# Kernel tuning notes

Measured on AMD Instinct MI355X. Metric: run time of the kernel, lower is better.

## Reference

```python
import jax, jax.numpy as jnp
import numpy as np

NUM_USERS = 100_000
NUM_ITEMS = 50_000
N_TOTAL = 150_100
EMBED_DIM = 64
NUM_LAYERS = 3
N_EDGES = 3_000_000
BATCH = 4096


def setup_inputs() -> dict:
    key = jax.random.key(0)
    k1, k2, k3, k4, k5, k6 = jax.random.split(key, 6)
    node_emb = jax.random.normal(k1, (N_TOTAL, EMBED_DIM), dtype=jnp.float32) * 0.1
    # COO sparse normalized adjacency (static irregular pattern)
    adj_row = jax.random.randint(k2, (N_EDGES,), 0, N_TOTAL, dtype=jnp.int32)
    adj_col = jax.random.randint(k3, (N_EDGES,), 0, N_TOTAL, dtype=jnp.int32)
    adj_val = jax.random.uniform(k4, (N_EDGES,), dtype=jnp.float32) * 0.05
    user_ids = jax.random.randint(k5, (BATCH,), 0, NUM_USERS, dtype=jnp.int32)
    item_ids = jax.random.randint(k6, (BATCH,), 0, NUM_ITEMS, dtype=jnp.int32)
    return {"node_emb": node_emb, "adj_val": adj_val, "adj_row": adj_row,
            "adj_col": adj_col, "user_ids": user_ids, "item_ids": item_ids}


def reference(node_emb, adj_val, adj_row, adj_col, user_ids, item_ids):
    # LightGCN propagation: K sparse SpMM layers, running mean over K+1 embeddings
    emb = node_emb                       # [N, D] layer-0
    acc = emb                            # running sum instead of stack+mean
    for _ in range(NUM_LAYERS):
        # SpMM: out[r] += val * emb[c]   (COO scatter-add)
        msgs = adj_val[:, None] * emb[adj_col]          # [E, D]
        emb = jax.ops.segment_sum(msgs, adj_row, num_segments=N_TOTAL)
        acc = acc + emb
    final = acc / jnp.float32(NUM_LAYERS + 1)           # mean over layers
    users = final[:NUM_USERS]
    items = final[NUM_USERS:NUM_USERS + NUM_ITEMS]
    u = users[user_ids]                                 # [B, D]
    i = items[item_ids]                                 # [B, D]
    return (u * i).sum(axis=-1)                         # [B]
```

## Files before the change

kernel.cpp:

```cpp
#include <hip/hip_runtime.h>

#define N_TOTAL    150100
#define NUM_USERS  100000
#define DIM        64
#define BSHIFT     8
#define BROWS      (1 << BSHIFT)
#define NBUK       ((N_TOTAL + BROWS - 1) / BROWS)
#define EPB        4096
#define CAP        5632
#define RSP        260

#define VSCALE     262144.0f
#define VINV       (1.0f / 262144.0f)

__device__ __forceinline__ int wave_incl_scan(int x, int lane) {
    #pragma unroll
    for (int off = 1; off < 64; off <<= 1) {
        int y = __shfl_up(x, off, 64);
        if (lane >= off) x += y;
    }
    return x;
}

__device__ __forceinline__ float ub0(unsigned w) { return (float)(w & 0xFFu); }
__device__ __forceinline__ float ub1(unsigned w) { return (float)((w >> 8) & 0xFFu); }
__device__ __forceinline__ float ub2(unsigned w) { return (float)((w >> 16) & 0xFFu); }
__device__ __forceinline__ float ub3(unsigned w) { return (float)(w >> 24); }

__device__ __forceinline__ unsigned quant_pack(float4 f, float inv) {
    int a = __float2int_rn(f.x * inv) + 128;
    int b = __float2int_rn(f.y * inv) + 128;
    int c = __float2int_rn(f.z * inv) + 128;
    int d = __float2int_rn(f.w * inv) + 128;
    a = min(max(a, 0), 255); b = min(max(b, 0), 255);
    c = min(max(c, 0), 255); d = min(max(d, 0), 255);
    return (unsigned)a | ((unsigned)b << 8) | ((unsigned)c << 16) | ((unsigned)d << 24);
}

__global__ void convert_quant(const float4* __restrict__ in4,
                              unsigned* __restrict__ q, float* __restrict__ sc,
                              int* __restrict__ gcount) {
    int t = blockIdx.x * blockDim.x + threadIdx.x;
    if (t < NBUK) gcount[t] = 0;
    int r = t >> 4, sl = t & 15;
    if (r >= N_TOTAL) return;
    float4 f = in4[(size_t)r * 16 + sl];
    float m = fmaxf(fmaxf(fabsf(f.x), fabsf(f.y)), fmaxf(fabsf(f.z), fabsf(f.w)));
    #pragma unroll
    for (int off = 1; off < 16; off <<= 1) m = fmaxf(m, __shfl_xor(m, off, 64));
    float inv = (m > 1e-30f) ? 127.0f / m : 0.0f;
    q[(size_t)r * 16 + sl] = quant_pack(f, inv);
    if (sl == 0) sc[r] = m * (1.0f / 127.0f);
}

__global__ void __launch_bounds__(256) fill_buckets(
        const int* __restrict__ rows, const int* __restrict__ cols,
        const float* __restrict__ vals, int n_edges,
        int* __restrict__ gcount,
        unsigned* __restrict__ epk, unsigned char* __restrict__ erow) {
    __shared__ unsigned      buf[EPB];
    __shared__ unsigned char rowb[EPB];
    __shared__ short         tgtb[EPB];
    __shared__ int hist[NBUK];
    __shared__ int pref[NBUK];
    __shared__ int cur[NBUK];
    __shared__ int loc[NBUK];
    __shared__ int wtot[4];
    const int tid = threadIdx.x;
    const int lane = tid & 63, wid = tid >> 6;
    const int base = blockIdx.x * EPB;
    int end = base + EPB; if (end > n_edges) end = n_edges;
    const int cnt = end - base;

    for (int i = tid; i < NBUK; i += 256) hist[i] = 0;
    __syncthreads();
    for (int i = base + tid; i < end; i += 256)
        atomicAdd(&hist[rows[i] >> BSHIFT], 1);
    __syncthreads();
    for (int b = tid; b < NBUK; b += 256) {
        int h = hist[b];
        loc[b] = h ? atomicAdd(&gcount[b], h) : 0;
    }
    const int t0 = tid * 3;
    int t1 = t0 + 3; if (t1 > NBUK) t1 = NBUK;
    int s = 0;
    for (int i = t0; i < t1; ++i) s += hist[i];
    int incl = wave_incl_scan(s, lane);
    if (lane == 63) wtot[wid] = incl;
    __syncthreads();
    int wofs = 0;
    for (int w = 0; w < wid; ++w) wofs += wtot[w];
    int run = incl + wofs - s;
    for (int i = t0; i < t1; ++i) {
        int h = hist[i];
        pref[i] = run;
        cur[i] = run;
        run += h;
    }
    __syncthreads();
    for (int i = base + tid; i < end; i += 256) {
        int r = rows[i];
        int b = r >> BSHIFT;
        int pos = atomicAdd(&cur[b], 1);
        int q = (int)(vals[i] * VSCALE + 0.5f);
        if (q > 16383) q = 16383;
        buf[pos]  = ((unsigned)cols[i] << 14) | (unsigned)q;
        rowb[pos] = (unsigned char)(r & (BROWS - 1));
        tgtb[pos] = (short)b;
    }
    __syncthreads();
    for (int i = tid; i < cnt; i += 256) {
        int b = tgtb[i];
        int o = loc[b] + (i - pref[b]);
        if (o < CAP) {
            int g = b * CAP + o;
            epk[g]  = buf[i];
            erow[g] = rowb[i];
        }
    }
}

__global__ void __launch_bounds__(256) bucket_sort(
        unsigned* __restrict__ epk,
        const unsigned char* __restrict__ erow,
        const int* __restrict__ gcount,
        int* __restrict__ rs) {
    __shared__ unsigned buf[CAP];
    __shared__ int hist[BROWS];
    __shared__ int curl[BROWS];
    __shared__ int wtot[4];
    const int tid = threadIdx.x;
    const int lane = tid & 63, wid = tid >> 6;
    const int b = blockIdx.x;
    const int k0 = b * CAP;
    int cnt = gcount[b]; if (cnt > CAP) cnt = CAP;

    hist[tid] = 0;
    __syncthreads();
    for (int i = tid; i < cnt; i += 256) {
        buf[i] = epk[k0 + i];
        atomicAdd(&hist[erow[k0 + i]], 1);
    }
    __syncthreads();
    int s = hist[tid];
    int incl = wave_incl_scan(s, lane);
    if (lane == 63) wtot[wid] = incl;
    __syncthreads();
    int wofs = 0;
    for (int w = 0; w < wid; ++w) wofs += wtot[w];
    int ex = incl + wofs - s;
    const int rbase = b << BSHIFT;
    int nrow = N_TOTAL - rbase; if (nrow > BROWS) nrow = BROWS;
    if (tid < nrow) rs[b * RSP + tid] = k0 + ex;
    if (tid == 0) rs[b * RSP + nrow] = k0 + cnt;
    curl[tid] = ex;
    __syncthreads();
    for (int i = tid; i < cnt; i += 256) {
        int rl = erow[k0 + i];
        int pos = atomicAdd(&curl[rl], 1);
        epk[k0 + pos] = buf[i];
    }
}


__global__ void spmm_q8(const unsigned* __restrict__ qt,
                        const float* __restrict__ sc,
                        const int* __restrict__ rs,
                        const unsigned* __restrict__ epk,
                        unsigned* __restrict__ qo,
                        float* __restrict__ so) {
    int t = blockIdx.x * blockDim.x + threadIdx.x;
    int r = t >> 4;
    int sl = t & 15;
    int lane = threadIdx.x & 63;
    int subbase = lane & 48;
    if (r >= N_TOTAL) return;
    const int* rsb = rs + (r >> BSHIFT) * RSP + (r & (BROWS - 1));
    int k0 = rsb[0], k1 = rsb[1];
    float4 s = make_float4(0.f, 0.f, 0.f, 0.f);
    float corr = 0.f;
    for (int kb = k0; kb < k1; kb += 16) {
        int cnt = k1 - kb; if (cnt > 16) cnt = 16;
        unsigned pr = (sl < cnt) ? epk[kb + sl] : 0u;
        int j = 0;
        for (; j + 4 <= cnt; j += 4) {
            unsigned e0 = (unsigned)__shfl((int)pr, subbase + j + 0, 64);
            unsigned e1 = (unsigned)__shfl((int)pr, subbase + j + 1, 64);
            unsigned e2 = (unsigned)__shfl((int)pr, subbase + j + 2, 64);
            unsigned e3 = (unsigned)__shfl((int)pr, subbase + j + 3, 64);
            int c0 = e0 >> 14, c1 = e1 >> 14, c2 = e2 >> 14, c3 = e3 >> 14;
            unsigned w0 = qt[(size_t)c0 * 16 + sl];
            unsigned w1 = qt[(size_t)c1 * 16 + sl];
            unsigned w2 = qt[(size_t)c2 * 16 + sl];
            unsigned w3 = qt[(size_t)c3 * 16 + sl];
            float vs0 = (float)(e0 & 16383u) * VINV * sc[c0];
            float vs1 = (float)(e1 & 16383u) * VINV * sc[c1];
            float vs2 = (float)(e2 & 16383u) * VINV * sc[c2];
            float vs3 = (float)(e3 & 16383u) * VINV * sc[c3];
            corr += vs0 + vs1 + vs2 + vs3;
            s.x += vs0 * ub0(w0); s.y += vs0 * ub1(w0);
            s.z += vs0 * ub2(w0); s.w += vs0 * ub3(w0);
            s.x += vs1 * ub0(w1); s.y += vs1 * ub1(w1);
            s.z += vs1 * ub2(w1); s.w += vs1 * ub3(w1);
            s.x += vs2 * ub0(w2); s.y += vs2 * ub1(w2);
            s.z += vs2 * ub2(w2); s.w += vs2 * ub3(w2);
            s.x += vs3 * ub0(w3); s.y += vs3 * ub1(w3);
            s.z += vs3 * ub2(w3); s.w += vs3 * ub3(w3);
        }
        for (; j < cnt; ++j) {
            unsigned e = (unsigned)__shfl((int)pr, subbase + j, 64);
            int c = e >> 14;
            unsigned w = qt[(size_t)c * 16 + sl];
            float vs = (float)(e & 16383u) * VINV * sc[c];
            corr += vs;
            s.x += vs * ub0(w); s.y += vs * ub1(w);
            s.z += vs * ub2(w); s.w += vs * ub3(w);
        }
    }
    float c128 = 128.0f * corr;
    s.x -= c128; s.y -= c128; s.z -= c128; s.w -= c128;
    float m = fmaxf(fmaxf(fabsf(s.x), fabsf(s.y)), fmaxf(fabsf(s.z), fabsf(s.w)));
    #pragma unroll
    for (int off = 1; off < 16; off <<= 1) m = fmaxf(m, __shfl_xor(m, off, 64));
    float inv = (m > 1e-30f) ? 127.0f / m : 0.0f;
    qo[(size_t)r * 16 + sl] = quant_pack(s, inv);
    if (sl == 0) so[r] = m * (1.0f / 127.0f);
}

__device__ __forceinline__ float4 dec4(unsigned w, float s) {
    return make_float4(s * (ub0(w) - 128.0f), s * (ub1(w) - 128.0f),
                       s * (ub2(w) - 128.0f), s * (ub3(w) - 128.0f));
}

__device__ __forceinline__ float4 rowsum_q8(const unsigned* __restrict__ qt,
                                            const float* __restrict__ sc,
                                            const int* __restrict__ rs,
                                            const unsigned* __restrict__ epk,
                                            int r, int sl, int subbase) {
    const int* rsb = rs + (r >> BSHIFT) * RSP + (r & (BROWS - 1));
    int k0 = rsb[0], k1 = rsb[1];
    float4 s = make_float4(0.f, 0.f, 0.f, 0.f);
    float corr = 0.f;
    for (int kb = k0; kb < k1; kb += 16) {
        int cnt = k1 - kb; if (cnt > 16) cnt = 16;
        unsigned pr = (sl < cnt) ? epk[kb + sl] : 0u;
        for (int j = 0; j < cnt; ++j) {
            unsigned e = (unsigned)__shfl((int)pr, subbase + j, 64);
            int c = e >> 14;
            unsigned w = qt[(size_t)c * 16 + sl];
            float vs = (float)(e & 16383u) * VINV * sc[c];
            corr += vs;
            s.x += vs * ub0(w); s.y += vs * ub1(w);
            s.z += vs * ub2(w); s.w += vs * ub3(w);
        }
    }
    float c128 = 128.0f * corr;
    s.x -= c128; s.y -= c128; s.z -= c128; s.w -= c128;
    return s;
}

__global__ void final_dot_fused(const float4* __restrict__ emb4,
                                const unsigned* __restrict__ q1,
                                const float* __restrict__ s1,
                                const unsigned* __restrict__ q2,
                                const float* __restrict__ s2,
                                const int* __restrict__ rs,
                                const unsigned* __restrict__ epk,
                                const int* __restrict__ user_ids,
                                const int* __restrict__ item_ids,
                                float* __restrict__ out, int batch) {
    int t = blockIdx.x * blockDim.x + threadIdx.x;
    int b = t >> 4, sl = t & 15;
    int lane = threadIdx.x & 63;
    int subbase = lane & 48;
    if (b >= batch) return;
    int u = user_ids[b];
    int iN = NUM_USERS + item_ids[b];

    float4 lu = rowsum_q8(q2, s2, rs, epk, u, sl, subbase);
    float4 li = rowsum_q8(q2, s2, rs, epk, iN, sl, subbase);

    float4 nu = emb4[(size_t)u * 16 + sl];
    float4 au = dec4(q1[(size_t)u * 16 + sl], s1[u]);
    float4 bu = dec4(q2[(size_t)u * 16 + sl], s2[u]);
    float4 ni = emb4[(size_t)iN * 16 + sl];
    float4 ai = dec4(q1[(size_t)iN * 16 + sl], s1[iN]);
    float4 bi = dec4(q2[(size_t)iN * 16 + sl], s2[iN]);

    float ux = nu.x + au.x + bu.x + lu.x;
    float uy = nu.y + au.y + bu.y + lu.y;
    float uz = nu.z + au.z + bu.z + lu.z;
    float uw = nu.w + au.w + bu.w + lu.w;
    float ix = ni.x + ai.x + bi.x + li.x;
    float iy = ni.y + ai.y + bi.y + li.y;
    float iz = ni.z + ai.z + bi.z + li.z;
    float iw = ni.w + ai.w + bi.w + li.w;

    float s = ux * ix + uy * iy + uz * iz + uw * iw;
    #pragma unroll
    for (int off = 8; off > 0; off >>= 1) s += __shfl_down(s, off, 64);
    if (sl == 0) out[b] = s * (1.0f / 16.0f);
}


static inline size_t align256(size_t x) { return (x + 255) & ~(size_t)255; }

extern "C" void kernel_launch(void* const* d_in, const int* in_sizes, int n_in,
                              void* d_out, int out_size, void* d_ws, size_t ws_size,
                              hipStream_t stream) {
    const float* node_emb = (const float*)d_in[0];
    const float* adj_val  = (const float*)d_in[1];
    const int*   adj_row  = (const int*)d_in[2];
    const int*   adj_col  = (const int*)d_in[3];
    const int*   user_ids = (const int*)d_in[4];
    const int*   item_ids = (const int*)d_in[5];
    float* out = (float*)d_out;

    const int n_edges = in_sizes[1];
    const int batch   = in_sizes[4];

    const size_t qtab_bytes = (size_t)N_TOTAL * 16 * sizeof(unsigned);
    const size_t sc_bytes   = (size_t)N_TOTAL * sizeof(float);

    char* p = (char*)d_ws;
    size_t off = 0;
    unsigned* q0 = (unsigned*)(p + off); off = align256(off + qtab_bytes);
    unsigned* q1 = (unsigned*)(p + off); off = align256(off + qtab_bytes);
    unsigned* q2 = (unsigned*)(p + off); off = align256(off + qtab_bytes);
    float* s0    = (float*)(p + off);    off = align256(off + sc_bytes);
    float* s1    = (float*)(p + off);    off = align256(off + sc_bytes);
    float* s2    = (float*)(p + off);    off = align256(off + sc_bytes);
    int* gcount  = (int*)(p + off);      off = align256(off + (size_t)NBUK * sizeof(int));
    int* rs      = (int*)(p + off);      off = align256(off + (size_t)NBUK * RSP * sizeof(int));
    unsigned* epk = (unsigned*)(p + off); off = align256(off + (size_t)NBUK * CAP * sizeof(unsigned));
    unsigned char* erow = (unsigned char*)(p + off); off = align256(off + (size_t)NBUK * CAP);
    (void)ws_size;

    const int nbf = (n_edges + EPB - 1) / EPB;
    const int rblocks = ((N_TOTAL * 16) + 255) / 256;

    convert_quant<<<rblocks, 256, 0, stream>>>(
        (const float4*)node_emb, q0, s0, gcount);

    fill_buckets<<<nbf, 256, 0, stream>>>(adj_row, adj_col, adj_val, n_edges,
                                          gcount, epk, erow);
    bucket_sort<<<NBUK, 256, 0, stream>>>(epk, erow, gcount, rs);

    spmm_q8<<<rblocks, 256, 0, stream>>>(q0, s0, rs, epk, q1, s1);
    spmm_q8<<<rblocks, 256, 0, stream>>>(q1, s1, rs, epk, q2, s2);

    {
        int threads = batch * 16;
        final_dot_fused<<<(threads + 255) / 256, 256, 0, stream>>>(
            (const float4*)node_emb, q1, s1, q2, s2, rs, epk,
            user_ids, item_ids, out, batch);
    }
}
```

Before: 303.6 us.

## Vectorize edge loading in fill_buckets and pack payload with row byte

fill_buckets now reads rows, cols and vals once, using 128-bit vector loads, and holds 16 edges per thread in registers instead of reading rows twice from global memory. The packed payload and the local row byte are written together as one uint2 into a single bucket array, which replaces separate byte writes to erow. bucket_sort reads the combined entries and writes the sorted 32-bit payloads back into the same buffer, with rs offsets rescaled to that view. This trades more registers per thread and a larger intermediate buffer for fewer global passes and coalesced loads.

```diff
diff --git a/kernel.cpp b/kernel.cpp
--- a/kernel.cpp
+++ b/kernel.cpp
@@ -7,6 +7,7 @@
 #define BROWS      (1 << BSHIFT)
 #define NBUK       ((N_TOTAL + BROWS - 1) / BROWS)
 #define EPB        4096
+#define EPT        16
 #define CAP        5632
 #define RSP        260
 
@@ -53,12 +54,12 @@
     if (sl == 0) sc[r] = m * (1.0f / 127.0f);
 }
 
-__global__ void __launch_bounds__(256) fill_buckets(
+__global__ void __launch_bounds__(256, 4) fill_buckets(
         const int* __restrict__ rows, const int* __restrict__ cols,
         const float* __restrict__ vals, int n_edges,
         int* __restrict__ gcount,
-        unsigned* __restrict__ epk, unsigned char* __restrict__ erow) {
-    __shared__ unsigned      buf[EPB];
+        uint2* __restrict__ epk8) {
+    __shared__ unsigned      payb[EPB];
     __shared__ unsigned char rowb[EPB];
     __shared__ short         tgtb[EPB];
     __shared__ int hist[NBUK];
@@ -73,10 +74,54 @@
     const int cnt = end - base;
 
     for (int i = tid; i < NBUK; i += 256) hist[i] = 0;
-    __syncthreads();
-    for (int i = base + tid; i < end; i += 256)
-        atomicAdd(&hist[rows[i] >> BSHIFT], 1);
-    __syncthreads();
+
+    unsigned pay[EPT];
+    unsigned er[EPT];
+    __syncthreads();
+
+    if (cnt == EPB) {
+        #pragma unroll
+        for (int g = 0; g < 4; ++g) {
+            const int e = base + (g * 256 + tid) * 4;
+            int4   r4 = *(const int4*)(rows + e);
+            int4   c4 = *(const int4*)(cols + e);
+            float4 v4 = *(const float4*)(vals + e);
+            int rr[4] = { r4.x, r4.y, r4.z, r4.w };
+            int cc[4] = { c4.x, c4.y, c4.z, c4.w };
+            float vv[4] = { v4.x, v4.y, v4.z, v4.w };
+            #pragma unroll
+            for (int k = 0; k < 4; ++k) {
+                const int j = g * 4 + k;
+                int q = (int)(vv[k] * VSCALE + 0.5f);
+                if (q > 16383) q = 16383;
+                pay[j] = ((unsigned)cc[k] << 14) | (unsigned)q;
+                er[j]  = (unsigned)rr[k];
+                atomicAdd(&hist[rr[k] >> BSHIFT], 1);
+            }
+        }
+    } else {
+        #pragma unroll
+        for (int g = 0; g < 4; ++g) {
+            const int e0 = base + (g * 256 + tid) * 4;
+            #pragma unroll
+            for (int k = 0; k < 4; ++k) {
+                const int j = g * 4 + k;
+                const int e = e0 + k;
+                if (e < end) {
+                    int r = rows[e];
+                    int q = (int)(vals[e] * VSCALE + 0.5f);
+                    if (q > 16383) q = 16383;
+                    pay[j] = ((unsigned)cols[e] << 14) | (unsigned)q;
+                    er[j]  = (unsigned)r;
+                    atomicAdd(&hist[r >> BSHIFT], 1);
+                } else {
+                    er[j] = 0xFFFFFFFFu;
+                }
+            }
+        }
+    }
+    __syncthreads();
+
     for (int b = tid; b < NBUK; b += 256) {
         int h = hist[b];
         loc[b] = h ? atomicAdd(&gcount[b], h) : 0;
@@ -98,48 +143,51 @@
         run += h;
     }
     __syncthreads();
-    for (int i = base + tid; i < end; i += 256) {
-        int r = rows[i];
-        int b = r >> BSHIFT;
-        int pos = atomicAdd(&cur[b], 1);
-        int q = (int)(vals[i] * VSCALE + 0.5f);
-        if (q > 16383) q = 16383;
-        buf[pos]  = ((unsigned)cols[i] << 14) | (unsigned)q;
-        rowb[pos] = (unsigned char)(r & (BROWS - 1));
-        tgtb[pos] = (short)b;
-    }
-    __syncthreads();
+
+    #pragma unroll
+    for (int j = 0; j < EPT; ++j) {
+        unsigned r = er[j];
+        if (r != 0xFFFFFFFFu) {
+            int b = (int)(r >> BSHIFT);
+            int pos = atomicAdd(&cur[b], 1);
+            payb[pos] = pay[j];
+            rowb[pos] = (unsigned char)(r & (BROWS - 1));
+            tgtb[pos] = (short)b;
+        }
+    }
+    __syncthreads();
+
     for (int i = tid; i < cnt; i += 256) {
         int b = tgtb[i];
         int o = loc[b] + (i - pref[b]);
         if (o < CAP) {
-            int g = b * CAP + o;
-            epk[g]  = buf[i];
-            erow[g] = rowb[i];
+            epk8[(size_t)b * CAP + o] = make_uint2(payb[i], (unsigned)rowb[i]);
         }
     }
 }
 
 __global__ void __launch_bounds__(256) bucket_sort(
-        unsigned* __restrict__ epk,
-        const unsigned char* __restrict__ erow,
+        uint2* __restrict__ epk8,
         const int* __restrict__ gcount,
         int* __restrict__ rs) {
-    __shared__ unsigned buf[CAP];
+    __shared__ unsigned      buf[CAP];
+    __shared__ unsigned char rbuf[CAP];
     __shared__ int hist[BROWS];
     __shared__ int curl[BROWS];
     __shared__ int wtot[4];
     const int tid = threadIdx.x;
     const int lane = tid & 63, wid = tid >> 6;
     const int b = blockIdx.x;
-    const int k0 = b * CAP;
+    const size_t k0 = (size_t)b * CAP;
     int cnt = gcount[b]; if (cnt > CAP) cnt = CAP;
 
     hist[tid] = 0;
     __syncthreads();
     for (int i = tid; i < cnt; i += 256) {
-        buf[i] = epk[k0 + i];
-        atomicAdd(&hist[erow[k0 + i]], 1);
+        uint2 e = epk8[k0 + i];
+        buf[i]  = e.x;
+        rbuf[i] = (unsigned char)e.y;
+        atomicAdd(&hist[e.y & 255u], 1);
     }
     __syncthreads();
     int s = hist[tid];
@@ -151,14 +199,16 @@
     int ex = incl + wofs - s;
     const int rbase = b << BSHIFT;
     int nrow = N_TOTAL - rbase; if (nrow > BROWS) nrow = BROWS;
-    if (tid < nrow) rs[b * RSP + tid] = k0 + ex;
-    if (tid == 0) rs[b * RSP + nrow] = k0 + cnt;
+    const int o0 = 2 * b * CAP;
+    if (tid < nrow) rs[b * RSP + tid] = o0 + ex;
+    if (tid == 0) rs[b * RSP + nrow] = o0 + cnt;
     curl[tid] = ex;
     __syncthreads();
+    unsigned* out = (unsigned*)epk8;
     for (int i = tid; i < cnt; i += 256) {
-        int rl = erow[k0 + i];
+        int rl = rbuf[i];
         int pos = atomicAdd(&curl[rl], 1);
-        epk[k0 + pos] = buf[i];
+        out[o0 + pos] = buf[i];
     }
 }
 
@@ -332,8 +382,7 @@
     float* s2    = (float*)(p + off);    off = align256(off + sc_bytes);
     int* gcount  = (int*)(p + off);      off = align256(off + (size_t)NBUK * sizeof(int));
     int* rs      = (int*)(p + off);      off = align256(off + (size_t)NBUK * RSP * sizeof(int));
-    unsigned* epk = (unsigned*)(p + off); off = align256(off + (size_t)NBUK * CAP * sizeof(unsigned));
-    unsigned char* erow = (unsigned char*)(p + off); off = align256(off + (size_t)NBUK * CAP);
+    uint2* epk8  = (uint2*)(p + off);    off = align256(off + (size_t)NBUK * CAP * sizeof(uint2));
     (void)ws_size;
 
     const int nbf = (n_edges + EPB - 1) / EPB;
@@ -343,8 +392,10 @@
         (const float4*)node_emb, q0, s0, gcount);
 
     fill_buckets<<<nbf, 256, 0, stream>>>(adj_row, adj_col, adj_val, n_edges,
-                                          gcount, epk, erow);
-    bucket_sort<<<NBUK, 256, 0, stream>>>(epk, erow, gcount, rs);
+                                          gcount, epk8);
+    bucket_sort<<<NBUK, 256, 0, stream>>>(epk8, gcount, rs);
+
+    const unsigned* epk = (const unsigned*)epk8;
 
     spmm_q8<<<rblocks, 256, 0, stream>>>(q0, s0, rs, epk, q1, s1);
     spmm_q8<<<rblocks, 256, 0, stream>>>(q1, s1, rs, epk, q2, s2);
```

New measurement: 279.8 us. 1.09x faster.
